# Kernel tuning notes

Hardware: AMD Instinct MI355X
Metric: run time of the kernel (lower is better)

## Reference

```python
import jax, jax.numpy as jnp
import numpy as np

NP_, NG_ = 20000, 5000            # protein / go_annotation node counts
D_FEAT, D_HID, N_CLS = 512, 128, 1000
E_PP, E_PG, E_GP = 240000, 100000, 100000
NEG_SLOPE = -0.2                  # note: the repo default slope is negative
EPS = 1e-12


def _l2norm(x):
    n = jnp.linalg.norm(x, axis=1, keepdims=True)
    return x / jnp.maximum(n, EPS)


def _edge_softmax(logits, dst, n):
    # per-destination-node softmax over incoming edges, per feature channel
    m = jax.ops.segment_max(logits, dst, num_segments=n)
    e = jnp.exp(logits - m[dst])
    s = jax.ops.segment_sum(e, dst, num_segments=n)
    return e / s[dst]


def _type_attn(h_src, h_dst, src, dst, Wl, bl, Wr, br):
    # GCN-normalized aggregation onto dst nodes, then type-level attention logits,
    # broadcast back to edges (copy_u on the reversed relation graph).
    ns, nd = h_src.shape[0], h_dst.shape[0]
    ones = jnp.ones(src.shape[0], dtype=h_src.dtype)
    outdeg = jnp.clip(jax.ops.segment_sum(ones, src, num_segments=ns), 1.0)
    feat = h_src * (outdeg ** -0.5)[:, None]
    rst = jax.ops.segment_sum(feat[src], dst, num_segments=nd)
    indeg = jnp.clip(jax.ops.segment_sum(ones, dst, num_segments=nd), 1.0)
    rst = rst * (indeg ** -0.5)[:, None]
    ea = jax.nn.elu((h_dst @ Wl + bl) + (rst @ Wr + br))  # [nd, D_HID]
    return ea[dst]                                        # [E, D_HID]


def setup_inputs() -> dict:
    key = jax.random.key(0)
    ks = iter(jax.random.split(key, 40))

    def nrm(shape, s=0.05):
        return jax.random.normal(next(ks), shape, dtype=jnp.float32) * s

    def ri(n, hi):
        return jax.random.randint(next(ks), (n,), 0, hi, dtype=jnp.int32)

    zeros = lambda n: jnp.zeros((n,), jnp.float32)
    return dict(
        x_protein=jax.random.normal(next(ks), (NP_, D_FEAT), dtype=jnp.float32),
        x_go=jax.random.normal(next(ks), (NG_, N_CLS), dtype=jnp.float32),
        src_pp=ri(E_PP, NP_), dst_pp=ri(E_PP, NP_),
        src_pg=ri(E_PG, NP_), dst_pg=ri(E_PG, NG_),
        src_gp=ri(E_GP, NG_), dst_gp=ri(E_GP, NP_),
        W1p=nrm((D_FEAT, D_HID)), b1p=zeros(D_HID),
        W1g=nrm((N_CLS, D_HID)), b1g=zeros(D_HID),
        Wl_p=nrm((D_HID, D_HID)), bl_p=zeros(D_HID),
        Wl_g=nrm((D_HID, D_HID)), bl_g=zeros(D_HID),
        Wr_p=nrm((D_HID, D_HID)), br_p=zeros(D_HID),
        Wr_g=nrm((D_HID, D_HID)), br_g=zeros(D_HID),
        Wnl=nrm((D_HID, D_HID)), bnl=zeros(D_HID),
        Wnr=nrm((D_HID, D_HID)), bnr=zeros(D_HID),
        Wfc=nrm((D_HID, N_CLS)), bfc=zeros(N_CLS),
    )


def reference(x_protein, x_go, src_pp, dst_pp, src_pg, dst_pg, src_gp, dst_gp,
              W1p, b1p, W1g, b1g, Wl_p, bl_p, Wl_g, bl_g,
              Wr_p, br_p, Wr_g, br_g, Wnl, bnl, Wnr, bnr, Wfc, bfc):
    # input projection + row-wise l2 norm (dropout disabled / eval mode)
    hp = _l2norm(x_protein @ W1p + b1p)   # [NP, D_HID]
    hg = _l2norm(x_go @ W1g + b1g)        # [NG, D_HID]

    # ---- TypeAttention over each canonical etype ----
    a_pp = _type_attn(hp, hp, src_pp, dst_pp, Wl_p, bl_p, Wr_p, br_p)
    a_pg = _type_attn(hp, hg, src_pg, dst_pg, Wl_g, bl_g, Wr_p, br_p)
    a_gp = _type_attn(hg, hp, src_gp, dst_gp, Wl_p, bl_p, Wr_g, br_g)

    # homogeneous view: proteins [0,NP), go_annotation [NP,NP+NG)
    gsrc = jnp.concatenate([src_pp, src_pg, src_gp + NP_])
    gdst = jnp.concatenate([dst_pp, dst_pg + NP_, dst_gp])
    alpha = jnp.concatenate([a_pp, a_pg, a_gp], axis=0)   # [E, D_HID]
    n = NP_ + NG_
    alpha = _edge_softmax(alpha, gdst, n)

    # ---- NodeAttention on the homogeneous graph ----
    x = jnp.concatenate([hp, hg], axis=0)                 # [N, D_HID]
    hl = (x @ Wnl + bnl)[gsrc]
    hr = (x @ Wnr + bnr)[gdst]
    e = (hl + hr) * alpha
    e = jnp.where(e > 0, e, NEG_SLOPE * e)                # LeakyReLU(slope=-0.2)
    a = _edge_softmax(e, gdst, n)
    h = jax.ops.segment_sum(x[gsrc] * a, gdst, num_segments=n)

    out = h @ Wfc + bfc   # [N, N_CLS]; rows [:NP]=protein, [NP:]=go_annotation
    return out
```

## Files before the change

### kernel.cpp

```cpp
#include <hip/hip_runtime.h>
#include <math.h>

#define NP 20000
#define NG 5000
#define NTOT 25000
#define DF 512
#define NCLS 1000
#define DH 128
#define EPP 240000
#define EPG 100000
#define EGP 100000
#define ETOT 440000
#define FS 16
#define HB 16

typedef __attribute__((ext_vector_type(8))) __bf16 bf16x8;
typedef __attribute__((ext_vector_type(4))) float f32x4;

__device__ __forceinline__ void gl2lds16(const void* g, void* l) {
    __builtin_amdgcn_global_load_lds(
        (const __attribute__((address_space(1))) unsigned int*)g,
        (__attribute__((address_space(3))) unsigned int*)l, 16, 0, 0);
}

__device__ __forceinline__ float b2f(unsigned short u) {
    union { unsigned int i; float f; } c; c.i = ((unsigned int)u) << 16; return c.f;
}

__global__ __launch_bounds__(1024) void hist_part_kernel(
    const int* __restrict__ src_pp, const int* __restrict__ dst_pp,
    const int* __restrict__ src_pg, const int* __restrict__ dst_pg,
    const int* __restrict__ src_gp, const int* __restrict__ dst_gp,
    int* __restrict__ partial)
{
    __shared__ int bins[20000];
    const int job = blockIdx.y, b = blockIdx.x;
    const int* idx; int nbins, nedge; size_t pbase;
    switch (job) {
    case 0: idx = src_pp; nbins = 20000; nedge = EPP; pbase = 0;       break;
    case 1: idx = dst_pp; nbins = 20000; nedge = EPP; pbase = 320000;  break;
    case 2: idx = src_pg; nbins = 20000; nedge = EPG; pbase = 640000;  break;
    case 3: idx = dst_pg; nbins = 5000;  nedge = EPG; pbase = 960000;  break;
    case 4: idx = src_gp; nbins = 5000;  nedge = EGP; pbase = 1040000; break;
    default: idx = dst_gp; nbins = 20000; nedge = EGP; pbase = 1120000; break;
    }
    for (int i = threadIdx.x; i < nbins; i += 1024) bins[i] = 0;
    __syncthreads();
    const int chunk = (nedge + HB - 1) / HB;
    const int e0 = b * chunk, e1 = min(e0 + chunk, nedge);
    for (int e = e0 + threadIdx.x; e < e1; e += 1024) atomicAdd(&bins[idx[e]], 1);
    __syncthreads();
    int* dst = partial + pbase + (size_t)b * nbins;
    for (int i = threadIdx.x; i < nbins; i += 1024) dst[i] = bins[i];
}

__global__ __launch_bounds__(256) void hist_merge_kernel(const int* __restrict__ partial,
    int* __restrict__ outdeg_pp, int* __restrict__ indeg_pp,
    int* __restrict__ outdeg_pg, int* __restrict__ indeg_pg,
    int* __restrict__ outdeg_gp, int* __restrict__ indeg_gp,
    int* __restrict__ fill)
{
    const int job = blockIdx.y;
    const int bin = blockIdx.x * 256 + threadIdx.x;
    if (job == 6) {
        if (bin < NTOT * FS) fill[bin] = 0;
        return;
    }
    const int nbins = (job == 3 || job == 4) ? 5000 : 20000;
    if (bin >= nbins) return;
    size_t pbase; int* outp;
    switch (job) {
    case 0: pbase = 0;       outp = outdeg_pp; break;
    case 1: pbase = 320000;  outp = indeg_pp;  break;
    case 2: pbase = 640000;  outp = outdeg_pg; break;
    case 3: pbase = 960000;  outp = indeg_pg;  break;
    case 4: pbase = 1040000; outp = outdeg_gp; break;
    default: pbase = 1120000; outp = indeg_gp; break;
    }
    const int* p = partial + pbase + bin;
    int s = 0;
#pragma unroll
    for (int b = 0; b < HB; b++) s += p[(size_t)b * nbins];
    outp[bin] = s;
}

__global__ __launch_bounds__(1024) void scan_kernel(const int* __restrict__ indeg_pp,
                                                    const int* __restrict__ indeg_gp,
                                                    const int* __restrict__ indeg_pg,
                                                    int* __restrict__ row_ptr)
{
    __shared__ int part[1024];
    int t = threadIdx.x;
    const int CH = (NTOT + 1023) / 1024;
    int base = t * CH;
    auto cntf = [&](int idx) -> int {
        return (idx < NP) ? (indeg_pp[idx] + indeg_gp[idx]) : indeg_pg[idx - NP];
    };
    int s = 0;
    for (int i = 0; i < CH; i++) { int idx = base + i; if (idx < NTOT) s += cntf(idx); }
    part[t] = s;
    __syncthreads();
    for (int off = 1; off < 1024; off <<= 1) {
        int v = (t >= off) ? part[t - off] : 0;
        __syncthreads();
        part[t] += v;
        __syncthreads();
    }
    int run = (t == 0) ? 0 : part[t - 1];
    for (int i = 0; i < CH; i++) {
        int idx = base + i;
        if (idx < NTOT) { row_ptr[idx] = run; run += cntf(idx); }
    }
    if (t == 1023) row_ptr[NTOT] = part[1023];
}

__global__ void scatter_kernel(const int* __restrict__ src_pp, const int* __restrict__ dst_pp,
                               const int* __restrict__ src_pg, const int* __restrict__ dst_pg,
                               const int* __restrict__ src_gp, const int* __restrict__ dst_gp,
                               const int* __restrict__ outdeg_pp, const int* __restrict__ outdeg_pg,
                               const int* __restrict__ outdeg_gp,
                               const int* __restrict__ row_ptr, int* fill,
                               int2* __restrict__ edata)
{
    int e = blockIdx.x * blockDim.x + threadIdx.x;
    int s, d, t; float sc;
    if (e < EPP) {
        s = src_pp[e]; d = dst_pp[e]; t = 0;
        sc = rsqrtf((float)max(outdeg_pp[s], 1));
    } else if (e < EPP + EPG) {
        int i = e - EPP; s = src_pg[i]; d = NP + dst_pg[i]; t = 1;
        sc = rsqrtf((float)max(outdeg_pg[s], 1));
    } else if (e < ETOT) {
        int i = e - EPP - EPG; int sl = src_gp[i]; s = NP + sl; d = dst_gp[i]; t = 2;
        sc = rsqrtf((float)max(outdeg_gp[sl], 1));
    } else return;
    int pos = row_ptr[d] + atomicAdd(&fill[d * FS], 1);
    edata[pos] = make_int2(s | (t << 16), __float_as_int(sc));
}

__global__ __launch_bounds__(256) void conv_all_kernel(
    const float* __restrict__ xp, const float* __restrict__ xg,
    const float* W1p, const float* W1g, const float* Wlp, const float* Wrp, const float* Wrg,
    const float* Wnl, const float* Wnr, const float* Wfc,
    __bf16* __restrict__ xpb, __bf16* __restrict__ xgb,
    __bf16* w1pt, __bf16* w1gt, __bf16* wlpt, __bf16* wrpt, __bf16* wrgt,
    __bf16* wnlt, __bf16* wnrt, __bf16* wfct)
{
    const int b = blockIdx.x;
    if (b < 5008) {
        long long e = ((long long)b * 256 + threadIdx.x) * 8;
        int row = (int)(e >> 9), k = (int)(e & 511);
        __bf16 pk[8];
        if (row < NP) {
            f32x4 v0 = *(const f32x4*)(xp + (size_t)row * 512 + k);
            f32x4 v1 = *(const f32x4*)(xp + (size_t)row * 512 + k + 4);
#pragma unroll
            for (int i = 0; i < 4; i++) { pk[i] = (__bf16)v0[i]; pk[4 + i] = (__bf16)v1[i]; }
        } else {
#pragma unroll
            for (int i = 0; i < 8; i++) pk[i] = (__bf16)0.f;
        }
        *(bf16x8*)(xpb + e) = *(bf16x8*)pk;
        return;
    }
    if (b < 7536) {
        long long e = ((long long)(b - 5008) * 256 + threadIdx.x) * 8;
        int row = (int)(e >> 10), k = (int)(e & 1023);
        __bf16 pk[8];
        if (row < NG && k + 7 < 1000) {
            f32x4 v0 = *(const f32x4*)(xg + (size_t)row * 1000 + k);
            f32x4 v1 = *(const f32x4*)(xg + (size_t)row * 1000 + k + 4);
#pragma unroll
            for (int i = 0; i < 4; i++) { pk[i] = (__bf16)v0[i]; pk[4 + i] = (__bf16)v1[i]; }
        } else {
#pragma unroll
            for (int i = 0; i < 8; i++) {
                int kk = k + i;
                pk[i] = (__bf16)((row < NG && kk < 1000) ? xg[(size_t)row * 1000 + kk] : 0.f);
            }
        }
        *(bf16x8*)(xgb + e) = *(bf16x8*)pk;
        return;
    }
    int wb = b - 7536;
    int e;
    if (wb < 256)      { e = wb * 256 + threadIdx.x;          int n = e >> 9, k = e & 511;  w1pt[e] = (__bf16)W1p[(size_t)k * 128 + n]; }
    else if (wb < 768) { e = (wb - 256) * 256 + threadIdx.x;  int n = e >> 10, k = e & 1023; w1gt[e] = (__bf16)(k < 1000 ? W1g[(size_t)k * 128 + n] : 0.f); }
    else if (wb < 832) { e = (wb - 768) * 256 + threadIdx.x;  int n = e >> 7, k = e & 127;  wlpt[e] = (__bf16)Wlp[(size_t)k * 128 + n]; }
    else if (wb < 896) { e = (wb - 832) * 256 + threadIdx.x;  int n = e >> 7, k = e & 127;  wrpt[e] = (__bf16)Wrp[(size_t)k * 128 + n]; }
    else if (wb < 960) { e = (wb - 896) * 256 + threadIdx.x;  int n = e >> 7, k = e & 127;  wrgt[e] = (__bf16)Wrg[(size_t)k * 128 + n]; }
    else if (wb < 1024){ e = (wb - 960) * 256 + threadIdx.x;  int n = e >> 7, k = e & 127;  wnlt[e] = (__bf16)Wnl[(size_t)k * 128 + n]; }
    else if (wb < 1088){ e = (wb - 1024) * 256 + threadIdx.x; int n = e >> 7, k = e & 127;  wnrt[e] = (__bf16)Wnr[(size_t)k * 128 + n]; }
    else               { e = (wb - 1088) * 256 + threadIdx.x; int n = e >> 7, k = e & 127;  wfct[e] = (__bf16)(n < 1000 ? Wfc[(size_t)k * 1000 + n] : 0.f); }
}

struct GJob {
    const __bf16* A1;
    const __bf16* B1; const __bf16* B2;
    const float* b1; const float* b2;
    float* O1; __bf16* O2; __bf16* Ob;
    int M, N, Kp, ksteps;
};

template<int ACT, int DUALW, int EMIT>
__global__ __launch_bounds__(256) void gemm_bt(GJob j0, GJob j1, int split)
{
    __shared__ __align__(16) __bf16 As[64 * 32];
    __shared__ __align__(16) __bf16 Bs[128 * 32];
    __shared__ __align__(16) __bf16 B2s[DUALW ? 128 * 32 : 8];
    __shared__ float part[2][64];

    GJob j; int bx;
    if ((int)blockIdx.x < split) { j = j0; bx = blockIdx.x; }
    else { j = j1; bx = blockIdx.x - split; }

    const int tid = threadIdx.x;
    const int wave = tid >> 6, lane = tid & 63;
    const int wr = wave >> 1, wc = wave & 1;
    const int l15 = lane & 15, lh = lane >> 4;
    const int row0 = bx * 64;
    const int col0 = blockIdx.y * 128;

    const size_t aoff = (size_t)(row0 + (tid >> 2)) * j.Kp + (tid & 3) * 8;
    const size_t boff0 = (size_t)(col0 + (tid >> 2)) * j.Kp + (tid & 3) * 8;
    const size_t boff1 = boff0 + (size_t)64 * j.Kp;
    char* alds   = (char*)As + wave * 1024;
    char* blds0  = (char*)Bs + wave * 1024;
    char* blds1  = (char*)Bs + 4096 + wave * 1024;
    char* b2lds0 = (char*)B2s + wave * 1024;
    char* b2lds1 = (char*)B2s + 4096 + wave * 1024;

    f32x4 acc[2][4], acc2[2][4];
#pragma unroll
    for (int fm = 0; fm < 2; fm++)
#pragma unroll
        for (int fn = 0; fn < 4; fn++) {
            acc[fm][fn] = (f32x4)0.f;
            if (DUALW) acc2[fm][fn] = (f32x4)0.f;
        }

    for (int ks = 0; ks < j.ksteps; ks++) {
        const int k0 = ks * 32;
        __syncthreads();
        gl2lds16(j.A1 + aoff + k0, alds);
        gl2lds16(j.B1 + boff0 + k0, blds0);
        gl2lds16(j.B1 + boff1 + k0, blds1);
        if constexpr (DUALW) {
            gl2lds16(j.B2 + boff0 + k0, b2lds0);
            gl2lds16(j.B2 + boff1 + k0, b2lds1);
        }
        __syncthreads();

#pragma unroll
        for (int fm = 0; fm < 2; fm++) {
            bf16x8 a = *(const bf16x8*)&As[(wr * 32 + fm * 16 + l15) * 32 + lh * 8];
#pragma unroll
            for (int fn = 0; fn < 4; fn++) {
                bf16x8 b = *(const bf16x8*)&Bs[(wc * 64 + fn * 16 + l15) * 32 + lh * 8];
                acc[fm][fn] = __builtin_amdgcn_mfma_f32_16x16x32_bf16(a, b, acc[fm][fn], 0, 0, 0);
                if constexpr (DUALW) {
                    bf16x8 b2 = *(const bf16x8*)&B2s[(wc * 64 + fn * 16 + l15) * 32 + lh * 8];
                    acc2[fm][fn] = __builtin_amdgcn_mfma_f32_16x16x32_bf16(a, b2, acc2[fm][fn], 0, 0, 0);
                }
            }
        }
    }

    float bias[4], bias2[4];
#pragma unroll
    for (int fn = 0; fn < 4; fn++) {
        int col = col0 + wc * 64 + fn * 16 + l15;
        bias[fn] = 0.f; bias2[fn] = 0.f;
        if (col < j.N) {
            bias[fn] = j.b1[col];
            if (DUALW) bias2[fn] = j.b2[col];
        }
    }

    float vv[2][4][4];
#pragma unroll
    for (int fm = 0; fm < 2; fm++)
#pragma unroll
        for (int fn = 0; fn < 4; fn++)
#pragma unroll
            for (int r = 0; r < 4; r++) vv[fm][fn][r] = acc[fm][fn][r] + bias[fn];

    float scale[2][4];
#pragma unroll
    for (int fm = 0; fm < 2; fm++)
#pragma unroll
        for (int r = 0; r < 4; r++) scale[fm][r] = 1.f;

    if constexpr (ACT == 2) {
        float s[2][4];
#pragma unroll
        for (int fm = 0; fm < 2; fm++)
#pragma unroll
            for (int r = 0; r < 4; r++) {
                float v = 0.f;
#pragma unroll
                for (int fn = 0; fn < 4; fn++) v += vv[fm][fn][r] * vv[fm][fn][r];
                v += __shfl_xor(v, 1);
                v += __shfl_xor(v, 2);
                v += __shfl_xor(v, 4);
                v += __shfl_xor(v, 8);
                s[fm][r] = v;
            }
        __syncthreads();
        if (l15 == 0) {
#pragma unroll
            for (int fm = 0; fm < 2; fm++)
#pragma unroll
                for (int r = 0; r < 4; r++)
                    part[wc][wr * 32 + fm * 16 + lh * 4 + r] = s[fm][r];
        }
        __syncthreads();
#pragma unroll
        for (int fm = 0; fm < 2; fm++)
#pragma unroll
            for (int r = 0; r < 4; r++) {
                int rl = wr * 32 + fm * 16 + lh * 4 + r;
                float ss = part[0][rl] + part[1][rl];
                scale[fm][r] = 1.f / fmaxf(sqrtf(ss), 1e-12f);
            }
    }

#pragma unroll
    for (int fm = 0; fm < 2; fm++)
#pragma unroll
        for (int fn = 0; fn < 4; fn++)
#pragma unroll
            for (int r = 0; r < 4; r++) {
                int row = row0 + wr * 32 + fm * 16 + lh * 4 + r;
                int col = col0 + wc * 64 + fn * 16 + l15;
                if (row < j.M && col < j.N) {
                    float v = vv[fm][fn][r] * scale[fm][r];
                    if constexpr (EMIT == 0) j.O1[(size_t)row * j.N + col] = v;
                    if constexpr (EMIT == 2) j.Ob[(size_t)row * j.N + col] = (__bf16)v;
                    if constexpr (DUALW)
                        j.O2[(size_t)row * j.N + col] = (__bf16)(acc2[fm][fn][r] + bias2[fn]);
                }
            }
}

__global__ __launch_bounds__(256) void rst_hlr_kernel(
    const __bf16* __restrict__ xb,
    const int* __restrict__ row_ptr, const int2* __restrict__ edata,
    const int* __restrict__ indeg_pp, const int* __restrict__ indeg_gp,
    __bf16* __restrict__ rppb, __bf16* __restrict__ rgpb,
    const __bf16* __restrict__ wnlt, const __bf16* __restrict__ wnrt,
    const float* __restrict__ bnl, const float* __restrict__ bnr,
    __bf16* __restrict__ hlb, __bf16* __restrict__ hrb)
{
    __shared__ __align__(16) __bf16 As[64 * 32];
    __shared__ __align__(16) __bf16 Bs[128 * 32];
    __shared__ __align__(16) __bf16 B2s[128 * 32];

    const int tid = threadIdx.x;
    if (blockIdx.x < 10000) {
        const int d = blockIdx.x * 2 + (tid >> 7);
        const unsigned c = tid & 127;
        const int beg = row_ptr[d], end = row_ptr[d + 1];
        float spp = 0.f, sgp = 0.f;
        const unsigned short* xu = (const unsigned short*)xb;
        int i = beg;
        for (; i + 3 < end; i += 4) {
            int2 e0 = edata[i], e1 = edata[i + 1], e2 = edata[i + 2], e3 = edata[i + 3];
            float v0 = b2f(xu[(((unsigned)e0.x & 0xFFFFu) << 7) | c]) * __int_as_float(e0.y);
            float v1 = b2f(xu[(((unsigned)e1.x & 0xFFFFu) << 7) | c]) * __int_as_float(e1.y);
            float v2 = b2f(xu[(((unsigned)e2.x & 0xFFFFu) << 7) | c]) * __int_as_float(e2.y);
            float v3 = b2f(xu[(((unsigned)e3.x & 0xFFFFu) << 7) | c]) * __int_as_float(e3.y);
            if ((e0.x >> 16) == 0) spp += v0; else sgp += v0;
            if ((e1.x >> 16) == 0) spp += v1; else sgp += v1;
            if ((e2.x >> 16) == 0) spp += v2; else sgp += v2;
            if ((e3.x >> 16) == 0) spp += v3; else sgp += v3;
        }
        for (; i < end; i++) {
            int2 e0 = edata[i];
            float v0 = b2f(xu[(((unsigned)e0.x & 0xFFFFu) << 7) | c]) * __int_as_float(e0.y);
            if ((e0.x >> 16) == 0) spp += v0; else sgp += v0;
        }
        float ipp = rsqrtf((float)max(indeg_pp[d], 1));
        float igp = rsqrtf((float)max(indeg_gp[d], 1));
        rppb[((size_t)d << 7) | c] = (__bf16)(spp * ipp);
        rgpb[((size_t)d << 7) | c] = (__bf16)(sgp * igp);
        return;
    }

    const int bx = blockIdx.x - 10000;
    const int wave = tid >> 6, lane = tid & 63;
    const int wr = wave >> 1, wc = wave & 1;
    const int l15 = lane & 15, lh = lane >> 4;
    const int row0 = bx * 64;

    const size_t aoff = (size_t)(row0 + (tid >> 2)) * 128 + (tid & 3) * 8;
    const size_t boff0 = (size_t)(tid >> 2) * 128 + (tid & 3) * 8;
    const size_t boff1 = boff0 + (size_t)64 * 128;
    char* alds   = (char*)As + wave * 1024;
    char* blds0  = (char*)Bs + wave * 1024;
    char* blds1  = (char*)Bs + 4096 + wave * 1024;
    char* b2lds0 = (char*)B2s + wave * 1024;
    char* b2lds1 = (char*)B2s + 4096 + wave * 1024;

    f32x4 acc[2][4], acc2[2][4];
#pragma unroll
    for (int fm = 0; fm < 2; fm++)
#pragma unroll
        for (int fn = 0; fn < 4; fn++) { acc[fm][fn] = (f32x4)0.f; acc2[fm][fn] = (f32x4)0.f; }

    for (int ks = 0; ks < 4; ks++) {
        const int k0 = ks * 32;
        __syncthreads();
        gl2lds16(xb + aoff + k0, alds);
        gl2lds16(wnlt + boff0 + k0, blds0);
        gl2lds16(wnlt + boff1 + k0, blds1);
        gl2lds16(wnrt + boff0 + k0, b2lds0);
        gl2lds16(wnrt + boff1 + k0, b2lds1);
        __syncthreads();
#pragma unroll
        for (int fm = 0; fm < 2; fm++) {
            bf16x8 a = *(const bf16x8*)&As[(wr * 32 + fm * 16 + l15) * 32 + lh * 8];
#pragma unroll
            for (int fn = 0; fn < 4; fn++) {
                bf16x8 b  = *(const bf16x8*)&Bs[(wc * 64 + fn * 16 + l15) * 32 + lh * 8];
                bf16x8 b2 = *(const bf16x8*)&B2s[(wc * 64 + fn * 16 + l15) * 32 + lh * 8];
                acc[fm][fn]  = __builtin_amdgcn_mfma_f32_16x16x32_bf16(a, b,  acc[fm][fn],  0, 0, 0);
                acc2[fm][fn] = __builtin_amdgcn_mfma_f32_16x16x32_bf16(a, b2, acc2[fm][fn], 0, 0, 0);
            }
        }
    }

#pragma unroll
    for (int fn = 0; fn < 4; fn++) {
        int col = wc * 64 + fn * 16 + l15;
        float bl = bnl[col], br = bnr[col];
#pragma unroll
        for (int fm = 0; fm < 2; fm++)
#pragma unroll
            for (int r = 0; r < 4; r++) {
                int row = row0 + wr * 32 + fm * 16 + lh * 4 + r;
                if (row < NTOT) {
                    hlb[(size_t)row * DH + col] = (__bf16)(acc[fm][fn][r] + bl);
                    hrb[(size_t)row * DH + col] = (__bf16)(acc2[fm][fn][r] + br);
                }
            }
    }
}

__global__ __launch_bounds__(256) void ea_wa_kernel(
    const __bf16* __restrict__ xb, const __bf16* __restrict__ rppb, const __bf16* __restrict__ rgpb,
    const __bf16* __restrict__ wl, const __bf16* __restrict__ wrp, const __bf16* __restrict__ wrg,
    const float* __restrict__ blp, const float* __restrict__ brp, const float* __restrict__ brg,
    const int* __restrict__ indeg_pp, const int* __restrict__ indeg_gp,
    float* __restrict__ wpp, float* __restrict__ wgp)
{
    __shared__ __align__(16) __bf16 A1s[64 * 32], A2s[64 * 32], A3s[64 * 32];
    __shared__ __align__(16) __bf16 B1s[128 * 32], B2s[128 * 32], B3s[128 * 32];

    const int tid = threadIdx.x;
    const int wave = tid >> 6, lane = tid & 63;
    const int wr = wave >> 1, wc = wave & 1;
    const int l15 = lane & 15, lh = lane >> 4;
    const int row0 = blockIdx.x * 64;

    const size_t aoff = (size_t)(row0 + (tid >> 2)) * 128 + (tid & 3) * 8;
    const size_t boff0 = (size_t)(tid >> 2) * 128 + (tid & 3) * 8;
    const size_t boff1 = boff0 + (size_t)64 * 128;
    char* a1 = (char*)A1s + wave * 1024;
    char* a2 = (char*)A2s + wave * 1024;
    char* a3 = (char*)A3s + wave * 1024;
    char* b1l0 = (char*)B1s + wave * 1024, *b1l1 = (char*)B1s + 4096 + wave * 1024;
    char* b2l0 = (char*)B2s + wave * 1024, *b2l1 = (char*)B2s + 4096 + wave * 1024;
    char* b3l0 = (char*)B3s + wave * 1024, *b3l1 = (char*)B3s + 4096 + wave * 1024;

    f32x4 accL[2][4], accP[2][4], accG[2][4];
#pragma unroll
    for (int fm = 0; fm < 2; fm++)
#pragma unroll
        for (int fn = 0; fn < 4; fn++) {
            accL[fm][fn] = (f32x4)0.f; accP[fm][fn] = (f32x4)0.f; accG[fm][fn] = (f32x4)0.f;
        }

    for (int ks = 0; ks < 4; ks++) {
        const int k0 = ks * 32;
        __syncthreads();
        gl2lds16(xb + aoff + k0, a1);
        gl2lds16(rppb + aoff + k0, a2);
        gl2lds16(rgpb + aoff + k0, a3);
        gl2lds16(wl + boff0 + k0, b1l0);  gl2lds16(wl + boff1 + k0, b1l1);
        gl2lds16(wrp + boff0 + k0, b2l0); gl2lds16(wrp + boff1 + k0, b2l1);
        gl2lds16(wrg + boff0 + k0, b3l0); gl2lds16(wrg + boff1 + k0, b3l1);
        __syncthreads();

#pragma unroll
        for (int fm = 0; fm < 2; fm++) {
            const int arow = (wr * 32 + fm * 16 + l15) * 32 + lh * 8;
            bf16x8 aL = *(const bf16x8*)&A1s[arow];
            bf16x8 aP = *(const bf16x8*)&A2s[arow];
            bf16x8 aG = *(const bf16x8*)&A3s[arow];
#pragma unroll
            for (int fn = 0; fn < 4; fn++) {
                const int brow = (wc * 64 + fn * 16 + l15) * 32 + lh * 8;
                bf16x8 bL = *(const bf16x8*)&B1s[brow];
                bf16x8 bP = *(const bf16x8*)&B2s[brow];
                bf16x8 bG = *(const bf16x8*)&B3s[brow];
                accL[fm][fn] = __builtin_amdgcn_mfma_f32_16x16x32_bf16(aL, bL, accL[fm][fn], 0, 0, 0);
                accP[fm][fn] = __builtin_amdgcn_mfma_f32_16x16x32_bf16(aP, bP, accP[fm][fn], 0, 0, 0);
                accG[fm][fn] = __builtin_amdgcn_mfma_f32_16x16x32_bf16(aG, bG, accG[fm][fn], 0, 0, 0);
            }
        }
    }

    float bp[4], bg[4];
#pragma unroll
    for (int fn = 0; fn < 4; fn++) {
        int col = wc * 64 + fn * 16 + l15;
        bp[fn] = blp[col] + brp[col];
        bg[fn] = blp[col] + brg[col];
    }

#pragma unroll
    for (int fm = 0; fm < 2; fm++)
#pragma unroll
        for (int r = 0; r < 4; r++) {
            int row = row0 + wr * 32 + fm * 16 + lh * 4 + r;
            int rr = min(row, NP - 1);
            int npp = indeg_pp[rr], ngp = indeg_gp[rr];
#pragma unroll
            for (int fn = 0; fn < 4; fn++) {
                int col = wc * 64 + fn * 16 + l15;
                float app = accL[fm][fn][r] + accP[fm][fn][r] + bp[fn];
                app = app > 0.f ? app : (__expf(app) - 1.f);
                float agp = accL[fm][fn][r] + accG[fm][fn][r] + bg[fn];
                agp = agp > 0.f ? agp : (__expf(agp) - 1.f);
                float wppv = 0.f, wgpv = 0.f;
                if (npp > 0 && ngp > 0) {
                    float mx = fmaxf(app, agp);
                    float ep = __expf(app - mx), eg = __expf(agp - mx);
                    float den = (float)npp * ep + (float)ngp * eg;
                    wppv = ep / den; wgpv = eg / den;
                } else if (npp > 0) wppv = 1.f / (float)npp;
                else if (ngp > 0) wgpv = 1.f / (float)ngp;
                if (row < NP) {
                    wpp[(size_t)row * DH + col] = wppv;
                    wgp[(size_t)row * DH + col] = wgpv;
                }
            }
        }
}

__global__ __launch_bounds__(256) void pack_xhl_kernel(const unsigned int* __restrict__ xb2,
                                                       const unsigned int* __restrict__ hl2,
                                                       uint4* __restrict__ xhl4)
{
    int i = blockIdx.x * 256 + threadIdx.x;
    if (i >= 25024 * 128 / 4) return;
    unsigned int xa = xb2[i * 2], xbv = xb2[i * 2 + 1];
    unsigned int ha = hl2[i * 2], hbv = hl2[i * 2 + 1];
    uint4 o;
    o.x = (xa & 0xFFFFu) | (ha << 16);
    o.y = (xa >> 16) | (hbv & 0u) | (ha & 0xFFFF0000u);
    o.y = (xa >> 16) | (ha & 0xFFFF0000u);
    o.z = (xbv & 0xFFFFu) | (hbv << 16);
    o.w = (xbv >> 16) | (hbv & 0xFFFF0000u);
    xhl4[i] = o;
}

__global__ __launch_bounds__(128) void node_attn_kernel(const unsigned int* __restrict__ xhl,
                                                        const __bf16* __restrict__ hrb,
                                                        const float* __restrict__ wpp_arr,
                                                        const float* __restrict__ wgp_arr,
                                                        const int* __restrict__ indeg_pg,
                                                        const int* __restrict__ row_ptr,
                                                        const int2* __restrict__ edata,
                                                        __bf16* __restrict__ hb)
{
    const int d = blockIdx.x;
    const unsigned c = threadIdx.x;
    const int beg = row_ptr[d], end = row_ptr[d + 1];
    const float hrd = b2f(((const unsigned short*)hrb)[((size_t)d << 7) | c]);
    float wppv, wgpv;
    if (d < NP) {
        wppv = wpp_arr[((size_t)d << 7) | c];
        wgpv = wgp_arr[((size_t)d << 7) | c];
    } else {
        float w = 1.f / (float)max(indeg_pg[d - NP], 1);
        wppv = w; wgpv = w;
    }
    float ssum = 0.f, acc = 0.f;

    int i = beg;
    for (; i + 3 < end; i += 4) {
        int p0 = edata[i].x, p1 = edata[i + 1].x, p2 = edata[i + 2].x, p3 = edata[i + 3].x;
        unsigned int u0 = xhl[(((unsigned)p0 & 0xFFFFu) << 7) | c];
        unsigned int u1 = xhl[(((unsigned)p1 & 0xFFFFu) << 7) | c];
        unsigned int u2 = xhl[(((unsigned)p2 & 0xFFFFu) << 7) | c];
        unsigned int u3 = xhl[(((unsigned)p3 & 0xFFFFu) << 7) | c];
#pragma unroll
        for (int k = 0; k < 4; k++) {
            unsigned int u = (k == 0) ? u0 : (k == 1) ? u1 : (k == 2) ? u2 : u3;
            int p = (k == 0) ? p0 : (k == 1) ? p1 : (k == 2) ? p2 : p3;
            float xv  = __uint_as_float(u << 16);
            float hlv = __uint_as_float(u & 0xFFFF0000u);
            float al = ((p >> 16) == 0) ? wppv : wgpv;
            float e = (hlv + hrd) * al;
            e = fmaxf(e, -0.2f * e);
            float pw = __expf(e);
            ssum += pw;
            acc = fmaf(pw, xv, acc);
        }
    }
    for (; i < end; i++) {
        int p = edata[i].x;
        unsigned int u = xhl[(((unsigned)p & 0xFFFFu) << 7) | c];
        float xv  = __uint_as_float(u << 16);
        float hlv = __uint_as_float(u & 0xFFFF0000u);
        float al = ((p >> 16) == 0) ? wppv : wgpv;
        float e = (hlv + hrd) * al;
        e = fmaxf(e, -0.2f * e);
        float pw = __expf(e);
        ssum += pw;
        acc = fmaf(pw, xv, acc);
    }

    hb[((size_t)d << 7) | c] = (__bf16)((end > beg) ? acc / ssum : 0.f);
}

extern "C" void kernel_launch(void* const* d_in, const int* in_sizes, int n_in,
                              void* d_out, int out_size, void* d_ws, size_t ws_size,
                              hipStream_t stream)
{
    const float* x_protein = (const float*)d_in[0];
    const float* x_go      = (const float*)d_in[1];
    const int* src_pp = (const int*)d_in[2];
    const int* dst_pp = (const int*)d_in[3];
    const int* src_pg = (const int*)d_in[4];
    const int* dst_pg = (const int*)d_in[5];
    const int* src_gp = (const int*)d_in[6];
    const int* dst_gp = (const int*)d_in[7];
    const float* W1p = (const float*)d_in[8];
    const float* b1p = (const float*)d_in[9];
    const float* W1g = (const float*)d_in[10];
    const float* b1g = (const float*)d_in[11];
    const float* Wl_p = (const float*)d_in[12];
    const float* bl_p = (const float*)d_in[13];
    const float* Wr_p = (const float*)d_in[16];
    const float* br_p = (const float*)d_in[17];
    const float* Wr_g = (const float*)d_in[18];
    const float* br_g = (const float*)d_in[19];
    const float* Wnl = (const float*)d_in[20];
    const float* bnl = (const float*)d_in[21];
    const float* Wnr = (const float*)d_in[22];
    const float* bnr = (const float*)d_in[23];
    const float* Wfc = (const float*)d_in[24];
    const float* bfc = (const float*)d_in[25];
    float* out = (float*)d_out;

    size_t off = 0;
    char* base = (char*)d_ws;
    auto alloc = [&](size_t words) { void* p = base + off * 4; off += (words + 7) & ~(size_t)7; return p; };

    __bf16* xb  = (__bf16*)alloc((size_t)25024 * 128 / 2);
    __bf16* hlb = (__bf16*)alloc((size_t)25024 * 128 / 2);
    __bf16* hrb = (__bf16*)alloc((size_t)25024 * 128 / 2);
    char* U = (char*)alloc((size_t)25024 * 128);
    __bf16* rppb = (__bf16*)U;
    __bf16* rgpb = (__bf16*)(U + (size_t)20032 * 128 * 2);
    unsigned int* xhl = (unsigned int*)U;
    char* R1 = (char*)alloc((size_t)5128192 + 2588672);
    int*    partial = (int*)R1;
    __bf16* xpb = (__bf16*)R1;
    __bf16* xgb = (__bf16*)(R1 + (size_t)20032 * 512 * 2);
    float*  wpp = (float*)R1;
    float*  wgp = wpp + (size_t)20000 * 128;
    __bf16* haggb = (__bf16*)(wgp + (size_t)20000 * 128);
    __bf16* w1pt = (__bf16*)alloc(128 * 512 / 2);
    __bf16* w1gt = (__bf16*)alloc(128 * 1024 / 2);
    __bf16* wlpt = (__bf16*)alloc(128 * 128 / 2);
    __bf16* wrpt = (__bf16*)alloc(128 * 128 / 2);
    __bf16* wrgt = (__bf16*)alloc(128 * 128 / 2);
    __bf16* wnlt = (__bf16*)alloc(128 * 128 / 2);
    __bf16* wnrt = (__bf16*)alloc(128 * 128 / 2);
    __bf16* wfct = (__bf16*)alloc(1024 * 128 / 2);
    int* outdeg_pp = (int*)alloc(NP);
    int* outdeg_pg = (int*)alloc(NP);
    int* outdeg_gp = (int*)alloc(NG);
    int* indeg_pp  = (int*)alloc(NP);
    int* indeg_gp  = (int*)alloc(NP);
    int* indeg_pg  = (int*)alloc(NG);
    int* fill      = (int*)alloc((size_t)NTOT * FS);
    int* row_ptr   = (int*)alloc(NTOT + 1);
    int2* edata    = (int2*)alloc((size_t)ETOT * 2);

    hist_part_kernel<<<dim3(HB, 6), 1024, 0, stream>>>(
        src_pp, dst_pp, src_pg, dst_pg, src_gp, dst_gp, partial);
    hist_merge_kernel<<<dim3((NTOT * FS + 255) / 256, 7), 256, 0, stream>>>(
        partial, outdeg_pp, indeg_pp, outdeg_pg, indeg_pg, outdeg_gp, indeg_gp, fill);
    scan_kernel<<<1, 1024, 0, stream>>>(indeg_pp, indeg_gp, indeg_pg, row_ptr);
    scatter_kernel<<<(ETOT + 255) / 256, 256, 0, stream>>>(
        src_pp, dst_pp, src_pg, dst_pg, src_gp, dst_gp,
        outdeg_pp, outdeg_pg, outdeg_gp, row_ptr, fill, edata);
    conv_all_kernel<<<9136, 256, 0, stream>>>(
        x_protein, x_go, W1p, W1g, Wl_p, Wr_p, Wr_g, Wnl, Wnr, Wfc,
        xpb, xgb, w1pt, w1gt, wlpt, wrpt, wrgt, wnlt, wnrt, wfct);

    {
        GJob p0 = { xpb, w1pt, nullptr, b1p, nullptr, nullptr, nullptr, xb, NP, 128, 512, 16 };
        GJob p1 = { xgb, w1gt, nullptr, b1g, nullptr, nullptr, nullptr,
                    xb + (size_t)NP * 128, NG, 128, 1024, 32 };
        gemm_bt<2, 0, 2><<<392, 256, 0, stream>>>(p0, p1, 313);
    }

    rst_hlr_kernel<<<10391, 256, 0, stream>>>(
        xb, row_ptr, edata, indeg_pp, indeg_gp, rppb, rgpb,
        wnlt, wnrt, bnl, bnr, hlb, hrb);

    ea_wa_kernel<<<313, 256, 0, stream>>>(xb, rppb, rgpb, wlpt, wrpt, wrgt,
                                          bl_p, br_p, br_g, indeg_pp, indeg_gp, wpp, wgp);

    pack_xhl_kernel<<<3128, 256, 0, stream>>>((const unsigned int*)xb, (const unsigned int*)hlb, (uint4*)xhl);

    node_attn_kernel<<<NTOT, 128, 0, stream>>>(xhl, hrb, wpp, wgp, indeg_pg, row_ptr, edata, haggb);

    {
        GJob o0 = { haggb, wfct, nullptr, bfc, nullptr, out, nullptr, nullptr, NTOT, NCLS, 128, 4 };
        gemm_bt<0, 0, 0><<<dim3(391, 8), 256, 0, stream>>>(o0, o0, 1 << 30);
    }

    (void)in_sizes; (void)n_in; (void)out_size; (void)ws_size;
}
```

Before: 295.6 us.

## Split fused rst/hlr kernel into packed-bf16 aggregation and dual-output GEMM

Replaces the combined kernel, which ran rst aggregation and the hl/hr projection GEMM as different block ranges of one launch, with two kernels. Aggregation now uses one 128-thread block per protein node: two half-blocks each take alternate edges, each lane loads a packed pair of bf16 channels, and the halves are reduced through shared memory. The hl/hr projection goes to the existing generic gemm_bt template in dual-weight mode. This halves the number of gather loads per edge and improves memory access width, at the cost of an extra kernel launch and a shared-memory reduction.

```diff
diff --git a/kernel.cpp b/kernel.cpp
--- a/kernel.cpp
+++ b/kernel.cpp
@@ -341,110 +341,6 @@
                         j.O2[(size_t)row * j.N + col] = (__bf16)(acc2[fm][fn][r] + bias2[fn]);
                 }
             }
-}
-
-__global__ __launch_bounds__(256) void rst_hlr_kernel(
-    const __bf16* __restrict__ xb,
-    const int* __restrict__ row_ptr, const int2* __restrict__ edata,
-    const int* __restrict__ indeg_pp, const int* __restrict__ indeg_gp,
-    __bf16* __restrict__ rppb, __bf16* __restrict__ rgpb,
-    const __bf16* __restrict__ wnlt, const __bf16* __restrict__ wnrt,
-    const float* __restrict__ bnl, const float* __restrict__ bnr,
-    __bf16* __restrict__ hlb, __bf16* __restrict__ hrb)
-{
-    __shared__ __align__(16) __bf16 As[64 * 32];
-    __shared__ __align__(16) __bf16 Bs[128 * 32];
-    __shared__ __align__(16) __bf16 B2s[128 * 32];
-
-    const int tid = threadIdx.x;
-    if (blockIdx.x < 10000) {
-        const int d = blockIdx.x * 2 + (tid >> 7);
-        const unsigned c = tid & 127;
-        const int beg = row_ptr[d], end = row_ptr[d + 1];
-        float spp = 0.f, sgp = 0.f;
-        const unsigned short* xu = (const unsigned short*)xb;
-        int i = beg;
-        for (; i + 3 < end; i += 4) {
-            int2 e0 = edata[i], e1 = edata[i + 1], e2 = edata[i + 2], e3 = edata[i + 3];
-            float v0 = b2f(xu[(((unsigned)e0.x & 0xFFFFu) << 7) | c]) * __int_as_float(e0.y);
-            float v1 = b2f(xu[(((unsigned)e1.x & 0xFFFFu) << 7) | c]) * __int_as_float(e1.y);
-            float v2 = b2f(xu[(((unsigned)e2.x & 0xFFFFu) << 7) | c]) * __int_as_float(e2.y);
-            float v3 = b2f(xu[(((unsigned)e3.x & 0xFFFFu) << 7) | c]) * __int_as_float(e3.y);
-            if ((e0.x >> 16) == 0) spp += v0; else sgp += v0;
-            if ((e1.x >> 16) == 0) spp += v1; else sgp += v1;
-            if ((e2.x >> 16) == 0) spp += v2; else sgp += v2;
-            if ((e3.x >> 16) == 0) spp += v3; else sgp += v3;
-        }
-        for (; i < end; i++) {
-            int2 e0 = edata[i];
-            float v0 = b2f(xu[(((unsigned)e0.x & 0xFFFFu) << 7) | c]) * __int_as_float(e0.y);
-            if ((e0.x >> 16) == 0) spp += v0; else sgp += v0;
-        }
-        float ipp = rsqrtf((float)max(indeg_pp[d], 1));
-        float igp = rsqrtf((float)max(indeg_gp[d], 1));
-        rppb[((size_t)d << 7) | c] = (__bf16)(spp * ipp);
-        rgpb[((size_t)d << 7) | c] = (__bf16)(sgp * igp);
-        return;
-    }
-
-    const int bx = blockIdx.x - 10000;
-    const int wave = tid >> 6, lane = tid & 63;
-    const int wr = wave >> 1, wc = wave & 1;
-    const int l15 = lane & 15, lh = lane >> 4;
-    const int row0 = bx * 64;
-
-    const size_t aoff = (size_t)(row0 + (tid >> 2)) * 128 + (tid & 3) * 8;
-    const size_t boff0 = (size_t)(tid >> 2) * 128 + (tid & 3) * 8;
-    const size_t boff1 = boff0 + (size_t)64 * 128;
-    char* alds   = (char*)As + wave * 1024;
-    char* blds0  = (char*)Bs + wave * 1024;
-    char* blds1  = (char*)Bs + 4096 + wave * 1024;
-    char* b2lds0 = (char*)B2s + wave * 1024;
-    char* b2lds1 = (char*)B2s + 4096 + wave * 1024;
-
-    f32x4 acc[2][4], acc2[2][4];
-#pragma unroll
-    for (int fm = 0; fm < 2; fm++)
-#pragma unroll
-        for (int fn = 0; fn < 4; fn++) { acc[fm][fn] = (f32x4)0.f; acc2[fm][fn] = (f32x4)0.f; }
-
-    for (int ks = 0; ks < 4; ks++) {
-        const int k0 = ks * 32;
-        __syncthreads();
-        gl2lds16(xb + aoff + k0, alds);
-        gl2lds16(wnlt + boff0 + k0, blds0);
-        gl2lds16(wnlt + boff1 + k0, blds1);
-        gl2lds16(wnrt + boff0 + k0, b2lds0);
-        gl2lds16(wnrt + boff1 + k0, b2lds1);
-        __syncthreads();
-#pragma unroll
-        for (int fm = 0; fm < 2; fm++) {
-            bf16x8 a = *(const bf16x8*)&As[(wr * 32 + fm * 16 + l15) * 32 + lh * 8];
-#pragma unroll
-            for (int fn = 0; fn < 4; fn++) {
-                bf16x8 b  = *(const bf16x8*)&Bs[(wc * 64 + fn * 16 + l15) * 32 + lh * 8];
-                bf16x8 b2 = *(const bf16x8*)&B2s[(wc * 64 + fn * 16 + l15) * 32 + lh * 8];
-                acc[fm][fn]  = __builtin_amdgcn_mfma_f32_16x16x32_bf16(a, b,  acc[fm][fn],  0, 0, 0);
-                acc2[fm][fn] = __builtin_amdgcn_mfma_f32_16x16x32_bf16(a, b2, acc2[fm][fn], 0, 0, 0);
-            }
-        }
-    }
-
-#pragma unroll
-    for (int fn = 0; fn < 4; fn++) {
-        int col = wc * 64 + fn * 16 + l15;
-        float bl = bnl[col], br = bnr[col];
-#pragma unroll
-        for (int fm = 0; fm < 2; fm++)
-#pragma unroll
-            for (int r = 0; r < 4; r++) {
-                int row = row0 + wr * 32 + fm * 16 + lh * 4 + r;
-                if (row < NTOT) {
-                    hlb[(size_t)row * DH + col] = (__bf16)(acc[fm][fn][r] + bl);
-                    hrb[(size_t)row * DH + col] = (__bf16)(acc2[fm][fn][r] + br);
-                }
-            }
-    }
 }
 
 __global__ __launch_bounds__(256) void ea_wa_kernel(
@@ -549,6 +445,64 @@
         }
 }
 
+__global__ __launch_bounds__(128) void rst_agg_kernel(const __bf16* __restrict__ x,
+                                                      const int* __restrict__ row_ptr,
+                                                      const int2* __restrict__ edata,
+                                                      const int* __restrict__ indeg_pp,
+                                                      const int* __restrict__ indeg_gp,
+                                                      __bf16* __restrict__ rppb, __bf16* __restrict__ rgpb)
+{
+    const int d = blockIdx.x;
+    const int tid = threadIdx.x;
+    const unsigned c2 = tid & 63;
+    const int h = tid >> 6;
+    const int beg = row_ptr[d], end = row_ptr[d + 1];
+    const unsigned int* xu = (const unsigned int*)x;
+    float spp0 = 0.f, spp1 = 0.f, sgp0 = 0.f, sgp1 = 0.f;
+
+    int i = beg + h;
+    for (; i + 6 < end; i += 8) {
+        int2 e0 = edata[i], e1 = edata[i + 2], e2 = edata[i + 4], e3 = edata[i + 6];
+        unsigned u0 = xu[(((unsigned)e0.x & 0xFFFFu) << 6) | c2];
+        unsigned u1 = xu[(((unsigned)e1.x & 0xFFFFu) << 6) | c2];
+        unsigned u2 = xu[(((unsigned)e2.x & 0xFFFFu) << 6) | c2];
+        unsigned u3 = xu[(((unsigned)e3.x & 0xFFFFu) << 6) | c2];
+#pragma unroll
+        for (int k = 0; k < 4; k++) {
+            unsigned u = (k == 0) ? u0 : (k == 1) ? u1 : (k == 2) ? u2 : u3;
+            int2 e = (k == 0) ? e0 : (k == 1) ? e1 : (k == 2) ? e2 : e3;
+            float lo = __uint_as_float(u << 16);
+            float hi = __uint_as_float(u & 0xFFFF0000u);
+            float sc = __int_as_float(e.y);
+            if ((e.x >> 16) == 0) { spp0 = fmaf(lo, sc, spp0); spp1 = fmaf(hi, sc, spp1); }
+            else                  { sgp0 = fmaf(lo, sc, sgp0); sgp1 = fmaf(hi, sc, sgp1); }
+        }
+    }
+    for (; i < end; i += 2) {
+        int2 e = edata[i];
+        unsigned u = xu[(((unsigned)e.x & 0xFFFFu) << 6) | c2];
+        float lo = __uint_as_float(u << 16);
+        float hi = __uint_as_float(u & 0xFFFF0000u);
+        float sc = __int_as_float(e.y);
+        if ((e.x >> 16) == 0) { spp0 = fmaf(lo, sc, spp0); spp1 = fmaf(hi, sc, spp1); }
+        else                  { sgp0 = fmaf(lo, sc, sgp0); sgp1 = fmaf(hi, sc, sgp1); }
+    }
+
+    __shared__ float red[4][64];
+    if (h == 1) { red[0][c2] = spp0; red[1][c2] = spp1; red[2][c2] = sgp0; red[3][c2] = sgp1; }
+    __syncthreads();
+    if (h == 0) {
+        spp0 += red[0][c2]; spp1 += red[1][c2]; sgp0 += red[2][c2]; sgp1 += red[3][c2];
+        float ipp = rsqrtf((float)max(indeg_pp[d], 1));
+        float igp = rsqrtf((float)max(indeg_gp[d], 1));
+        union { unsigned u; __bf16 b[2]; } wp, wg;
+        wp.b[0] = (__bf16)(spp0 * ipp); wp.b[1] = (__bf16)(spp1 * ipp);
+        wg.b[0] = (__bf16)(sgp0 * igp); wg.b[1] = (__bf16)(sgp1 * igp);
+        ((unsigned*)rppb)[((unsigned)d << 6) | c2] = wp.u;
+        ((unsigned*)rgpb)[((unsigned)d << 6) | c2] = wg.u;
+    }
+}
+
 __global__ __launch_bounds__(256) void pack_xhl_kernel(const unsigned int* __restrict__ xb2,
                                                        const unsigned int* __restrict__ hl2,
                                                        uint4* __restrict__ xhl4)
@@ -559,7 +513,6 @@
     unsigned int ha = hl2[i * 2], hbv = hl2[i * 2 + 1];
     uint4 o;
     o.x = (xa & 0xFFFFu) | (ha << 16);
-    o.y = (xa >> 16) | (hbv & 0u) | (ha & 0xFFFF0000u);
     o.y = (xa >> 16) | (ha & 0xFFFF0000u);
     o.z = (xbv & 0xFFFFu) | (hbv << 16);
     o.w = (xbv >> 16) | (hbv & 0xFFFF0000u);
@@ -711,9 +664,12 @@
         gemm_bt<2, 0, 2><<<392, 256, 0, stream>>>(p0, p1, 313);
     }
 
-    rst_hlr_kernel<<<10391, 256, 0, stream>>>(
-        xb, row_ptr, edata, indeg_pp, indeg_gp, rppb, rgpb,
-        wnlt, wnrt, bnl, bnr, hlb, hrb);
+    rst_agg_kernel<<<NP, 128, 0, stream>>>(xb, row_ptr, edata, indeg_pp, indeg_gp, rppb, rgpb);
+
+    {
+        GJob h0 = { xb, wnlt, wnrt, bnl, bnr, nullptr, hrb, hlb, NTOT, 128, 128, 4 };
+        gemm_bt<0, 1, 2><<<391, 256, 0, stream>>>(h0, h0, 1 << 30);
+    }
 
     ea_wa_kernel<<<313, 256, 0, stream>>>(xb, rppb, rgpb, wlpt, wrpt, wrgt,
                                           bl_p, br_p, br_g, indeg_pp, indeg_gp, wpp, wgp);
```

Measured after the change: 257.8 us. 1.15x faster.
